# Performance work log

Measured on AMD Instinct MI355X. Metric: run time of the kernel, lower is better.

Reference implementation:

```python
import jax, jax.numpy as jnp
import numpy as np

B, S, H = 8, 512, 1024          # batch, seq_len, hidden_size
T, K, FF = 8, 2, 4096           # num_thoughts, top_k, ffn dim (4*H)
NH = 8                          # combiner attention heads
HD = H // NH
CREATIVITY = 1.0


def setup_inputs() -> dict:
    key = jax.random.key(0)
    ks = jax.random.split(key, 16)
    s = 0.02
    return {
        "hidden_states": jax.random.normal(ks[0], (B, S, H), jnp.float32),
        # router
        "router_w": jax.random.normal(ks[1], (H, T), jnp.float32) * s,
        "router_b": jnp.zeros((T,), jnp.float32),
        # thought branch FFNs (one per thought)
        "W1": jax.random.normal(ks[2], (T, H, FF), jnp.float32) * s,
        "b1": jnp.zeros((T, FF), jnp.float32),
        "W2": jax.random.normal(ks[3], (T, FF, H), jnp.float32) * s,
        "b2": jnp.zeros((T, H), jnp.float32),
        # attention combiner (MultiheadAttention proj weights)
        "Wq": jax.random.normal(ks[4], (H, H), jnp.float32) * s,
        "bq": jnp.zeros((H,), jnp.float32),
        "Wk": jax.random.normal(ks[5], (H, H), jnp.float32) * s,
        "bk": jnp.zeros((H,), jnp.float32),
        "Wv": jax.random.normal(ks[6], (H, H), jnp.float32) * s,
        "bv": jnp.zeros((H,), jnp.float32),
        "Wo": jax.random.normal(ks[7], (H, H), jnp.float32) * s,
        "bo": jnp.zeros((H,), jnp.float32),
    }


def reference(hidden_states, router_w, router_b, W1, b1, W2, b2,
              Wq, bq, Wk, bk, Wv, bv, Wo, bo):
    # ---- router: mean-pool -> linear -> softmax -> top-k ----
    pooled = hidden_states.mean(axis=1)                       # [B,H]
    router_probs = jax.nn.softmax(pooled @ router_w + router_b, axis=-1)  # [B,T]
    top_p, top_i = jax.lax.top_k(router_probs, K)             # [B,K]
    weights = jax.nn.softmax(top_p, axis=-1)                  # renormalized active weights [B,K]

    # ---- grouped branch FFN (gather expert weights, batched GEMMs) ----
    h = jnp.einsum('bsh,bkhf->bksf', hidden_states, W1[top_i]) + b1[top_i][:, :, None, :]
    h = jax.nn.gelu(h, approximate=False)
    branch_out = jnp.einsum('bksf,bkfh->bksh', h, W2[top_i]) + b2[top_i][:, :, None, :]
    branch_out = branch_out * CREATIVITY                      # [B,K,S,H]

    # ---- attention combiner over flattened thoughts [B, K*S, H] ----
    L = K * S
    flat = branch_out.reshape(B, L, H)
    q = (flat @ Wq + bq).reshape(B, L, NH, HD)
    k = (flat @ Wk + bk).reshape(B, L, NH, HD)
    v = (flat @ Wv + bv).reshape(B, L, NH, HD)
    scores = jnp.einsum('blhd,bmhd->bhlm', q, k) / jnp.sqrt(jnp.float32(HD))
    attn = jax.nn.softmax(scores, axis=-1)
    ctx = jnp.einsum('bhlm,bmhd->blhd', attn, v).reshape(B, L, H)
    attended = (ctx @ Wo + bo).reshape(B, K, S, H)

    combined = jnp.einsum('bksh,bk->bsh', attended, weights)  # [B,S,H]

    # ---- metrics ----
    entropy = jnp.mean(-jnp.sum(router_probs * jnp.log(router_probs + 1e-8), axis=1))
    a = branch_out[:, 0].reshape(B, -1)
    b_ = branch_out[:, 1].reshape(B, -1)
    cos = jnp.sum(a * b_, -1) / jnp.maximum(
        jnp.linalg.norm(a, axis=-1) * jnp.linalg.norm(b_, axis=-1), 1e-8)
    diversity = jnp.mean(1.0 - cos)
    return combined, entropy, diversity
```

## Files before the change

kernel.cpp:

```cpp
#include <hip/hip_runtime.h>
#include <hip/hip_bf16.h>
#include <math.h>

typedef float f32x4 __attribute__((ext_vector_type(4)));
typedef short s16x8 __attribute__((ext_vector_type(8)));
typedef short s16x4 __attribute__((ext_vector_type(4)));
typedef unsigned int u32;

#define DEVI __device__ __forceinline__

#define Bn   8
#define Sn   512
#define Hn   1024
#define Tn   8
#define Kn   2
#define FFn  4096
#define NHn  8
#define HDn  128
#define Ln   1024
#define OUT_COMBINED 4194304

DEVI unsigned short f2bf(float x) {
  __hip_bfloat16 h = __float2bfloat16(x);
  union { __hip_bfloat16 h; unsigned short u; } cv; cv.h = h; return cv.u;
}
DEVI float bf2f(unsigned short u) {
  union { u32 i; float f; } cv; cv.i = ((u32)u) << 16; return cv.f;
}

typedef __attribute__((address_space(3))) u32 lds_u32;
typedef __attribute__((address_space(1))) u32 glb_u32;
DEVI void gload16(const void* g, void* l) {
  __builtin_amdgcn_global_load_lds((const glb_u32*)g, (lds_u32*)l, 16, 0, 0);
}

__global__ __launch_bounds__(256) void pool_part_k(const float* __restrict__ hid, float* __restrict__ part)
{
  const int b = blockIdx.x, scn = blockIdx.y;
  const int hh = threadIdx.x * 4;
  float4 acc = make_float4(0.f, 0.f, 0.f, 0.f);
  const float* base = hid + ((long)b * Sn + (long)scn * 128) * Hn + hh;
  for (int s = 0; s < 128; ++s) {
    float4 v = *(const float4*)(base + (long)s * Hn);
    acc.x += v.x; acc.y += v.y; acc.z += v.z; acc.w += v.w;
  }
  *(float4*)(part + ((long)(scn * Bn + b)) * Hn + hh) = acc;
}

__global__ __launch_bounds__(256) void pool_final_k(const float* __restrict__ part, float* __restrict__ pooled)
{
  const int i = blockIdx.x * 256 + threadIdx.x;
  float s = 0.f;
  for (int sc = 0; sc < 4; ++sc) s += part[sc * (Bn * Hn) + i];
  pooled[i] = s * (1.f / (float)Sn);
}

__global__ __launch_bounds__(64) void router_k(
    const float* __restrict__ pooled, const float* __restrict__ rw, const float* __restrict__ rb,
    float* __restrict__ probs, int* __restrict__ topi, float* __restrict__ wts,
    int* __restrict__ flags, float* __restrict__ entropy_out)
{
  __shared__ float lg[64];
  __shared__ int sfl[8];
  __shared__ float sent[8];
  const int tid = threadIdx.x;
  const int b = tid >> 3, t = tid & 7;
  if (tid < 8) sfl[tid] = 0;
  float acc = rb[t];
  const float* pb = pooled + b * Hn;
  for (int i = 0; i < Hn; ++i) acc += pb[i] * rw[i * Tn + t];
  lg[tid] = acc;
  __syncthreads();
  if (t == 0) {
    float p[8];
    float mx = lg[b * 8];
    for (int i = 1; i < 8; ++i) mx = fmaxf(mx, lg[b * 8 + i]);
    float ssum = 0.f;
    for (int i = 0; i < 8; ++i) { p[i] = expf(lg[b * 8 + i] - mx); ssum += p[i]; }
    float ent = 0.f;
    for (int i = 0; i < 8; ++i) { p[i] /= ssum; ent -= p[i] * logf(p[i] + 1e-8f); probs[b * 8 + i] = p[i]; }
    sent[b] = ent;
    int i1 = 0;
    for (int i = 1; i < 8; ++i) if (p[i] > p[i1]) i1 = i;
    int i2 = (i1 == 0) ? 1 : 0;
    for (int i = 0; i < 8; ++i) if (i != i1 && p[i] > p[i2]) i2 = i;
    float w0 = 1.f / (1.f + expf(p[i2] - p[i1]));
    float w1 = 1.f / (1.f + expf(p[i1] - p[i2]));
    topi[b * 2] = i1; topi[b * 2 + 1] = i2;
    wts[b * 2] = w0; wts[b * 2 + 1] = w1;
    atomicOr(&sfl[i1], 1); atomicOr(&sfl[i2], 1);
  }
  __syncthreads();
  if (tid < 8) flags[tid] = sfl[tid];
  if (tid == 0) {
    float e = 0.f;
    for (int i = 0; i < 8; ++i) e += sent[i];
    entropy_out[0] = e * (1.f / (float)Bn);
  }
}

__global__ __launch_bounds__(256) void cvt_k(const float* __restrict__ in, unsigned short* __restrict__ out)
{
  const long i = ((long)blockIdx.x * 256 + threadIdx.x) * 4;
  float4 v = *(const float4*)(in + i);
  s16x4 o;
  o[0] = (short)f2bf(v.x); o[1] = (short)f2bf(v.y); o[2] = (short)f2bf(v.z); o[3] = (short)f2bf(v.w);
  *(s16x4*)(out + i) = o;
}

__global__ __launch_bounds__(256) void bias3_k(const float* __restrict__ bq, const float* __restrict__ bk,
                                               const float* __restrict__ bv, float* __restrict__ o)
{
  const int i = blockIdx.x * 256 + threadIdx.x;
  o[i] = bq[i]; o[i + 1024] = bk[i]; o[i + 2048] = bv[i];
}

__global__ __launch_bounds__(256) void transpose_k(const float* __restrict__ Win, unsigned short* __restrict__ Wout,
                                                   int Kd, int N, long sIn, long sOut, const int* __restrict__ flags)
{
  const int t = blockIdx.z;
  if (flags && flags[t] == 0) return;
  __shared__ float tile[64][65];
  const float* in = Win + (long)t * sIn;
  unsigned short* out = Wout + (long)t * sOut;
  const int kb = blockIdx.y * 64, nb = blockIdx.x * 64;
  const int tx = threadIdx.x & 15, ty = threadIdx.x >> 4;
  #pragma unroll
  for (int i = 0; i < 4; ++i) {
    const int r = ty + i * 16;
    float4 v = *(const float4*)(in + (long)(kb + r) * N + nb + tx * 4);
    tile[r][tx * 4 + 0] = v.x; tile[r][tx * 4 + 1] = v.y;
    tile[r][tx * 4 + 2] = v.z; tile[r][tx * 4 + 3] = v.w;
  }
  __syncthreads();
  #pragma unroll
  for (int i = 0; i < 4; ++i) {
    const int n = ty + i * 16;
    s16x4 o;
    #pragma unroll
    for (int j = 0; j < 4; ++j) o[j] = (short)f2bf(tile[tx * 4 + j][n]);
    *(s16x4*)(out + (long)(nb + n) * Kd + kb + tx * 4) = o;
  }
}

template<int EPI, int OUTMODE>
__global__ __launch_bounds__(256) void gemm_k(
    const unsigned short* __restrict__ A0, const unsigned short* __restrict__ Bt0,
    const float* __restrict__ bias0, unsigned short* __restrict__ C0,
    int N, int Kd,
    const int* __restrict__ topi, int kTop,
    long sA_b, long sA_p, long sBt_t, int sBias_t, long sC_p)
{
  __shared__ __align__(16) char smem[36864];
  const int z = blockIdx.z;
  const int bidx = kTop ? (z / kTop) : 0;
  const int t = topi ? topi[z] : 0;
  const unsigned short* A = A0 + (long)bidx * sA_b + (long)z * sA_p;
  const unsigned short* Bt = Bt0 + (long)t * sBt_t;
  const float* bias = bias0 + (long)t * sBias_t;
  unsigned short* C = C0 + (long)z * sC_p;

  const int m0 = blockIdx.y * 128;
  const int n0 = blockIdx.x * 128;
  const int tid = threadIdx.x;
  const int lane = tid & 63, w = tid >> 6;
  const int wm = w >> 1, wn = w & 1;

  const int srow = w * 32 + (lane >> 2);
  const int csw = ((lane & 3) ^ ((srow ^ (srow >> 2)) & 3)) << 4;

  const char* gA0 = (const char*)(A + (long)(m0 + srow) * Kd) + csw;
  const char* gA1 = (const char*)(A + (long)(m0 + srow + 16) * Kd) + csw;
  const char* gB0 = (const char*)(Bt + (long)(n0 + srow) * Kd) + csw;
  const char* gB1 = (const char*)(Bt + (long)(n0 + srow + 16) * Kd) + csw;

  char* ldsAw = smem + w * 2048;
  char* ldsBw = smem + 16384 + w * 2048;

  f32x4 acc[4][4];
  const f32x4 zero = {0.f, 0.f, 0.f, 0.f};
  #pragma unroll
  for (int i = 0; i < 4; ++i)
    #pragma unroll
    for (int j = 0; j < 4; ++j) acc[i][j] = zero;

  const int rA = lane & 15;
  const int cb = (lane >> 4) << 4;
  int aoff[4], boff[4];
  #pragma unroll
  for (int mi = 0; mi < 4; ++mi) {
    int row = wm * 64 + mi * 16 + rA;
    aoff[mi] = row * 64 + (cb ^ (((row ^ (row >> 2)) & 3) << 4));
    int rowb = wn * 64 + mi * 16 + rA;
    boff[mi] = rowb * 64 + (cb ^ (((rowb ^ (rowb >> 2)) & 3) << 4));
  }

  const int nIter = Kd >> 5;
  gload16(gA0, ldsAw);
  gload16(gA1, ldsAw + 1024);
  gload16(gB0, ldsBw);
  gload16(gB1, ldsBw + 1024);
  __syncthreads();

  int cur = 0;
  for (int it = 0; it < nIter; ++it) {
    if (it + 1 < nIter) {
      const long kb2 = (long)(it + 1) * 64;
      const int nb = cur ^ 1;
      gload16(gA0 + kb2, ldsAw + nb * 8192);
      gload16(gA1 + kb2, ldsAw + nb * 8192 + 1024);
      gload16(gB0 + kb2, ldsBw + nb * 8192);
      gload16(gB1 + kb2, ldsBw + nb * 8192 + 1024);
    }
    const char* pa = smem + cur * 8192;
    const char* pb = smem + 16384 + cur * 8192;
    s16x8 af[4], bfr[4];
    #pragma unroll
    for (int mi = 0; mi < 4; ++mi) af[mi] = *(const s16x8*)(pa + aoff[mi]);
    #pragma unroll
    for (int nj = 0; nj < 4; ++nj) bfr[nj] = *(const s16x8*)(pb + boff[nj]);
    __builtin_amdgcn_s_setprio(1);
    #pragma unroll
    for (int mi = 0; mi < 4; ++mi)
      #pragma unroll
      for (int nj = 0; nj < 4; ++nj)
        acc[mi][nj] = __builtin_amdgcn_mfma_f32_16x16x32_bf16(af[mi], bfr[nj], acc[mi][nj], 0, 0, 0);
    __builtin_amdgcn_s_setprio(0);
    __syncthreads();
    cur ^= 1;
  }

  unsigned short* et = (unsigned short*)(smem + w * 9216);
  const int r4 = (lane >> 4) << 2;
  const int nbase = n0 + wn * 64;
  const int seg = nbase >> 10;
  #pragma unroll
  for (int nj = 0; nj < 4; ++nj) {
    const int n = nbase + nj * 16 + rA;
    const float bv = bias[n];
    #pragma unroll
    for (int mi = 0; mi < 4; ++mi) {
      #pragma unroll
      for (int j = 0; j < 4; ++j) {
        float x = acc[mi][nj][j] + bv;
        if (EPI == 1) x = 0.5f * x * (1.0f + erff(x * 0.70710678118654752f));
        const int mrl = mi * 16 + r4 + j;
        const int ncl = nj * 16 + rA;
        if (OUTMODE == 0 || seg < 2) et[mrl * 72 + ncl] = f2bf(x);
        else                         et[ncl * 72 + mrl] = f2bf(x);
      }
    }
  }
  const int erow = lane >> 3, echunk = lane & 7;
  if (OUTMODE == 0) {
    const long r0 = m0 + wm * 64;
    #pragma unroll
    for (int rr = 0; rr < 8; ++rr) {
      const int row = rr * 8 + erow;
      s16x8 v = *(const s16x8*)(et + row * 72 + echunk * 8);
      *(s16x8*)(C + (r0 + row) * N + nbase + echunk * 8) = v;
    }
  } else {
    const int nseg = nbase & 1023;
    if (seg < 2) {
      unsigned short* dst = C + (long)seg * 8388608;
      const long r0 = m0 + wm * 64;
      #pragma unroll
      for (int rr = 0; rr < 8; ++rr) {
        const int row = rr * 8 + erow;
        s16x8 v = *(const s16x8*)(et + row * 72 + echunk * 8);
        *(s16x8*)(dst + (r0 + row) * 1024 + nseg + echunk * 8) = v;
      }
    } else {
      unsigned short* vtp = C + 16777216;
      const int bb = m0 >> 10;
      const int ltok0 = (m0 & 1023) + wm * 64;
      #pragma unroll
      for (int rr = 0; rr < 8; ++rr) {
        const int nrow = rr * 8 + erow;
        s16x8 v = *(const s16x8*)(et + nrow * 72 + echunk * 8);
        *(s16x8*)(vtp + ((long)(bb * 1024 + nseg + nrow)) * 1024 + ltok0 + echunk * 8) = v;
      }
    }
  }
}

__global__ __launch_bounds__(256) void flash_k(
    const unsigned short* __restrict__ q, const unsigned short* __restrict__ k,
    const unsigned short* __restrict__ vt, unsigned short* __restrict__ ctx)
{
  __shared__ unsigned short Ks[64 * 128];
  __shared__ unsigned short Vs[128 * 64];
  __shared__ unsigned short Ps[4][32 * 72];
  const int qt = blockIdx.x, h = blockIdx.y, b = blockIdx.z;
  const int tid = threadIdx.x, lane = tid & 63, w = tid >> 6;
  const int rA = lane & 15, g = lane >> 4;
  const int q0w = qt * 128 + w * 32;

  s16x8 qf[2][4];
  #pragma unroll
  for (int qi = 0; qi < 2; ++qi) {
    const unsigned short* qp = q + ((long)(b * Ln + q0w + qi * 16 + rA)) * Hn + h * HDn + g * 8;
    #pragma unroll
    for (int kk = 0; kk < 4; ++kk) qf[qi][kk] = *(const s16x8*)(qp + kk * 32);
  }

  f32x4 o[2][8];
  const f32x4 zero = {0.f, 0.f, 0.f, 0.f};
  #pragma unroll
  for (int qi = 0; qi < 2; ++qi)
    #pragma unroll
    for (int nn = 0; nn < 8; ++nn) o[qi][nn] = zero;
  float lrun[2][4];
  #pragma unroll
  for (int qi = 0; qi < 2; ++qi)
    #pragma unroll
    for (int j = 0; j < 4; ++j) lrun[qi][j] = 0.f;
  float m = 0.f;

  const float sc2 = 0.08838834764831845f * 1.4426950408889634f;

  const int krow0 = w * 16 + g;
  const int kc = lane & 15;
  const int vrow0 = w * 32 + (lane >> 3);
  const int vc = lane & 7;

  for (int kvt = 0; kvt < 16; ++kvt) {
    const int kv0 = kvt * 64;
    __syncthreads();
    #pragma unroll
    for (int qq = 0; qq < 4; ++qq) {
      const int rk = krow0 + qq * 4;
      gload16(k + ((long)(b * Ln + kv0 + rk)) * Hn + h * HDn + ((kc ^ (rk & 7)) * 8),
              (char*)Ks + w * 4096 + qq * 1024);
      const int rv = vrow0 + qq * 8;
      gload16(vt + ((long)(b * 1024 + h * HDn + rv)) * Ln + kv0 + ((vc ^ (rv & 7)) * 8),
              (char*)Vs + w * 4096 + qq * 1024);
    }
    __syncthreads();

    f32x4 sacc[2][4];
    #pragma unroll
    for (int qi = 0; qi < 2; ++qi)
      #pragma unroll
      for (int nj = 0; nj < 4; ++nj) sacc[qi][nj] = zero;
    #pragma unroll
    for (int kk = 0; kk < 4; ++kk) {
      #pragma unroll
      for (int nj = 0; nj < 4; ++nj) {
        const int row = nj * 16 + rA;
        const int byt = row * 256 + (((kk * 4 + g) ^ (row & 7)) << 4);
        s16x8 kf = *(const s16x8*)((const char*)Ks + byt);
        sacc[0][nj] = __builtin_amdgcn_mfma_f32_16x16x32_bf16(qf[0][kk], kf, sacc[0][nj], 0, 0, 0);
        sacc[1][nj] = __builtin_amdgcn_mfma_f32_16x16x32_bf16(qf[1][kk], kf, sacc[1][nj], 0, 0, 0);
      }
    }

    float vmax = -3.0e38f;
    #pragma unroll
    for (int qi = 0; qi < 2; ++qi)
      #pragma unroll
      for (int nj = 0; nj < 4; ++nj)
        #pragma unroll
        for (int j = 0; j < 4; ++j) {
          const float s = sacc[qi][nj][j] * sc2;
          sacc[qi][nj][j] = s;
          vmax = fmaxf(vmax, s);
        }
    if (!__all(vmax <= m + 8.0f)) {
      float mn = vmax;
      #pragma unroll
      for (int mm = 1; mm < 64; mm <<= 1) mn = fmaxf(mn, __shfl_xor(mn, mm, 64));
      const float al = exp2f(m - mn);
      #pragma unroll
      for (int qi = 0; qi < 2; ++qi) {
        #pragma unroll
        for (int nn = 0; nn < 8; ++nn)
          #pragma unroll
          for (int j = 0; j < 4; ++j) o[qi][nn][j] *= al;
        #pragma unroll
        for (int j = 0; j < 4; ++j) lrun[qi][j] *= al;
      }
      m = mn;
    }
    #pragma unroll
    for (int qi = 0; qi < 2; ++qi)
      #pragma unroll
      for (int j = 0; j < 4; ++j) {
        float p0 = exp2f(sacc[qi][0][j] - m);
        float p1 = exp2f(sacc[qi][1][j] - m);
        float p2 = exp2f(sacc[qi][2][j] - m);
        float p3 = exp2f(sacc[qi][3][j] - m);
        lrun[qi][j] += (p0 + p1) + (p2 + p3);
        const int prow = (qi * 16 + g * 4 + j) * 72;
        Ps[w][prow + 0 * 16 + rA] = f2bf(p0);
        Ps[w][prow + 1 * 16 + rA] = f2bf(p1);
        Ps[w][prow + 2 * 16 + rA] = f2bf(p2);
        Ps[w][prow + 3 * 16 + rA] = f2bf(p3);
      }

    s16x8 pf[2][2];
    #pragma unroll
    for (int qi = 0; qi < 2; ++qi)
      #pragma unroll
      for (int kk2 = 0; kk2 < 2; ++kk2)
        pf[qi][kk2] = *(const s16x8*)(&Ps[w][(qi * 16 + rA) * 72 + kk2 * 32 + g * 8]);
    #pragma unroll
    for (int kk2 = 0; kk2 < 2; ++kk2) {
      #pragma unroll
      for (int nn = 0; nn < 8; ++nn) {
        const int row = nn * 16 + rA;
        const int byt = row * 128 + (((kk2 * 4 + g) ^ (row & 7)) << 4);
        s16x8 vf = *(const s16x8*)((const char*)Vs + byt);
        o[0][nn] = __builtin_amdgcn_mfma_f32_16x16x32_bf16(pf[0][kk2], vf, o[0][nn], 0, 0, 0);
        o[1][nn] = __builtin_amdgcn_mfma_f32_16x16x32_bf16(pf[1][kk2], vf, o[1][nn], 0, 0, 0);
      }
    }
  }

  float linv[2][4];
  #pragma unroll
  for (int qi = 0; qi < 2; ++qi)
    #pragma unroll
    for (int j = 0; j < 4; ++j) {
      float l = lrun[qi][j];
      #pragma unroll
      for (int mm = 1; mm < 16; mm <<= 1) l += __shfl_xor(l, mm, 64);
      linv[qi][j] = 1.0f / l;
    }
  #pragma unroll
  for (int qi = 0; qi < 2; ++qi)
    #pragma unroll
    for (int nn = 0; nn < 8; ++nn)
      #pragma unroll
      for (int j = 0; j < 4; ++j) {
        const int row = q0w + qi * 16 + g * 4 + j;
        ctx[((long)(b * Ln + row)) * Hn + h * HDn + nn * 16 + rA] = f2bf(o[qi][nn][j] * linv[qi][j]);
      }
}

__global__ __launch_bounds__(256) void div_part_k(const unsigned short* __restrict__ br, float* __restrict__ part)
{
  const int b = blockIdx.y, ch = blockIdx.x;
  const unsigned short* a = br + (long)b * (2L * Sn * Hn);
  const unsigned short* c = a + (long)Sn * Hn;
  const int base = ch * 16384 + threadIdx.x * 8;
  float dot = 0.f, na = 0.f, nb = 0.f;
  #pragma unroll
  for (int i = 0; i < 8; ++i) {
    const int idx = base + i * 2048;
    s16x8 av = *(const s16x8*)(a + idx);
    s16x8 cv = *(const s16x8*)(c + idx);
    #pragma unroll
    for (int e = 0; e < 8; ++e) {
      float fa = bf2f((unsigned short)av[e]);
      float fc = bf2f((unsigned short)cv[e]);
      dot += fa * fc; na += fa * fa; nb += fc * fc;
    }
  }
  #pragma unroll
  for (int mm = 1; mm < 64; mm <<= 1) {
    dot += __shfl_xor(dot, mm, 64);
    na  += __shfl_xor(na, mm, 64);
    nb  += __shfl_xor(nb, mm, 64);
  }
  __shared__ float red[12];
  const int lane = threadIdx.x & 63, w = threadIdx.x >> 6;
  if (lane == 0) { red[w * 3] = dot; red[w * 3 + 1] = na; red[w * 3 + 2] = nb; }
  __syncthreads();
  if (threadIdx.x == 0) {
    float d = 0, x = 0, y = 0;
    for (int i = 0; i < 4; ++i) { d += red[i * 3]; x += red[i * 3 + 1]; y += red[i * 3 + 2]; }
    float* op = part + ((long)(b * 32 + ch)) * 3;
    op[0] = d; op[1] = x; op[2] = y;
  }
}

__global__ __launch_bounds__(64) void div_final_k(const float* __restrict__ part, float* __restrict__ outp)
{
  __shared__ float cosr[8];
  const int tid = threadIdx.x;
  if (tid < 8) {
    float d = 0, x = 0, y = 0;
    for (int i = 0; i < 32; ++i) {
      const float* p = part + ((long)(tid * 32 + i)) * 3;
      d += p[0]; x += p[1]; y += p[2];
    }
    cosr[tid] = d / fmaxf(sqrtf(x) * sqrtf(y), 1e-8f);
  }
  __syncthreads();
  if (tid == 0) {
    float s = 0.f;
    for (int i = 0; i < 8; ++i) s += 1.f - cosr[i];
    outp[0] = s * (1.f / 8.f);
  }
}

__global__ __launch_bounds__(256) void combine_k(const unsigned short* __restrict__ att,
                                                 const float* __restrict__ wts, float* __restrict__ out)
{
  const long i = ((long)blockIdx.x * 256 + threadIdx.x) * 8;
  const int b = (int)(i >> 19);
  const long rem = i & 524287;
  const unsigned short* a0 = att + (long)b * (2L * Sn * Hn) + rem;
  const unsigned short* a1 = a0 + (long)Sn * Hn;
  const float w0 = wts[b * 2], w1 = wts[b * 2 + 1];
  s16x8 v0 = *(const s16x8*)a0;
  s16x8 v1 = *(const s16x8*)a1;
  float r[8];
  #pragma unroll
  for (int e = 0; e < 8; ++e) r[e] = w0 * bf2f((unsigned short)v0[e]) + w1 * bf2f((unsigned short)v1[e]);
  *(float4*)(out + i)     = make_float4(r[0], r[1], r[2], r[3]);
  *(float4*)(out + i + 4) = make_float4(r[4], r[5], r[6], r[7]);
}

extern "C" void kernel_launch(void* const* d_in, const int* in_sizes, int n_in,
                              void* d_out, int out_size, void* d_ws, size_t ws_size,
                              hipStream_t stream)
{
  (void)in_sizes; (void)n_in; (void)out_size; (void)ws_size;
  const float* hidden   = (const float*)d_in[0];
  const float* router_w = (const float*)d_in[1];
  const float* router_b = (const float*)d_in[2];
  const float* W1 = (const float*)d_in[3];
  const float* b1 = (const float*)d_in[4];
  const float* W2 = (const float*)d_in[5];
  const float* b2 = (const float*)d_in[6];
  const float* Wq = (const float*)d_in[7];
  const float* bq = (const float*)d_in[8];
  const float* Wk = (const float*)d_in[9];
  const float* bk = (const float*)d_in[10];
  const float* Wv = (const float*)d_in[11];
  const float* bv = (const float*)d_in[12];
  const float* Wo = (const float*)d_in[13];
  const float* bo = (const float*)d_in[14];
  float* out = (float*)d_out;

  char* ws = (char*)d_ws;
  float* pooled  = (float*)(ws);
  float* ppart   = (float*)(ws + 32768);
  float* probs   = (float*)(ws + 163840);
  int*   topi    = (int*)  (ws + 164096);
  float* wts     = (float*)(ws + 164352);
  int*   flags   = (int*)  (ws + 164608);
  float* dpart   = (float*)(ws + 164864);
  float* qkvbias = (float*)(ws + 167936);
  unsigned short* hid_bf = (unsigned short*)(ws + 262144);
  unsigned short* Wt     = (unsigned short*)(ws + 262144 + 8388608);
  unsigned short* hbuf   = (unsigned short*)(ws + 262144 + 8388608 + 67108864);
  unsigned short* br     = (unsigned short*)(ws + 262144 + 8388608 + 134217728);
  unsigned short* wqkvo  = (unsigned short*)(ws + 262144 + 8388608 + 134217728 + 16777216);
  unsigned short* qb  = Wt;
  unsigned short* kbf = Wt + 8388608;
  unsigned short* vt  = Wt + 16777216;
  unsigned short* ctx = hbuf;
  unsigned short* att = hbuf + 8388608;
  unsigned short* wqt = wqkvo;
  unsigned short* wkt = wqkvo + 1048576;
  unsigned short* wvt = wqkvo + 2097152;
  unsigned short* wot = wqkvo + 3145728;

  pool_part_k<<<dim3(Bn, 4), 256, 0, stream>>>(hidden, ppart);
  pool_final_k<<<dim3(32), 256, 0, stream>>>(ppart, pooled);
  router_k<<<1, 64, 0, stream>>>(pooled, router_w, router_b, probs, topi, wts, flags, out + OUT_COMBINED);

  cvt_k<<<4096, 256, 0, stream>>>(hidden, hid_bf);
  bias3_k<<<4, 256, 0, stream>>>(bq, bk, bv, qkvbias);
  transpose_k<<<dim3(64, 16, Tn), 256, 0, stream>>>(W1, Wt, Hn, FFn, (long)Hn * FFn, (long)FFn * Hn, flags);
  transpose_k<<<dim3(16, 16, 1), 256, 0, stream>>>(Wq, wqt, Hn, Hn, 0, 0, nullptr);
  transpose_k<<<dim3(16, 16, 1), 256, 0, stream>>>(Wk, wkt, Hn, Hn, 0, 0, nullptr);
  transpose_k<<<dim3(16, 16, 1), 256, 0, stream>>>(Wv, wvt, Hn, Hn, 0, 0, nullptr);
  transpose_k<<<dim3(16, 16, 1), 256, 0, stream>>>(Wo, wot, Hn, Hn, 0, 0, nullptr);

  gemm_k<1, 0><<<dim3(FFn / 128, Sn / 128, 16), 256, 0, stream>>>(
      hid_bf, Wt, b1, hbuf, FFn, Hn, topi, 2,
      (long)Sn * Hn, 0L, (long)FFn * Hn, FFn, (long)Sn * FFn);

  transpose_k<<<dim3(16, 64, Tn), 256, 0, stream>>>(W2, Wt, FFn, Hn, (long)FFn * Hn, (long)Hn * FFn, flags);

  gemm_k<0, 0><<<dim3(Hn / 128, Sn / 128, 16), 256, 0, stream>>>(
      hbuf, Wt, b2, br, Hn, FFn, topi, 2,
      0L, (long)Sn * FFn, (long)Hn * FFn, Hn, (long)Sn * Hn);

  div_part_k<<<dim3(32, Bn), 256, 0, stream>>>(br, dpart);
  div_final_k<<<1, 64, 0, stream>>>(dpart, out + OUT_COMBINED + 1);

  gemm_k<0, 1><<<dim3(3072 / 128, (Bn * Ln) / 128, 1), 256, 0, stream>>>(
      br, wqkvo, qkvbias, qb, 3072, Hn, nullptr, 0, 0L, 0L, 0L, 0, 0L);

  flash_k<<<dim3(Ln / 128, NHn, Bn), 256, 0, stream>>>(qb, kbf, vt, ctx);

  gemm_k<0, 0><<<dim3(Hn / 128, (Bn * Ln) / 128, 1), 256, 0, stream>>>(
      ctx, wot, bo, att, Hn, Hn, nullptr, 0, 0L, 0L, 0L, 0, 0L);

  combine_k<<<2048, 256, 0, stream>>>(att, wts, out);
}
```

Measured before the change: 538.0 us.

## Replace 128x128 GEMM with 256-wide tiles and multi-stage LDS pipeline

Swaps the 128x128 double-buffered bf16 MFMA GEMM for a templated kernel with 256-wide N tiles and 256- or 128-row M tiles. It uses a 3-4 stage LDS ring with explicit vmcnt waits and global loads split across the two halves of each MFMA phase. The aim is more data reuse per tile and better overlap of memory with compute for the FFN, QKV and output GEMMs. The router's dot products are also split across 256 threads. In exchange, the larger tiles raise register and LDS use, and the hand-written waitcnt sequencing is fragile.

```diff
diff --git a/kernel.cpp b/kernel.cpp
--- a/kernel.cpp
+++ b/kernel.cpp
@@ -55,23 +55,27 @@
   pooled[i] = s * (1.f / (float)Sn);
 }
 
-__global__ __launch_bounds__(64) void router_k(
+__global__ __launch_bounds__(256) void router_k(
     const float* __restrict__ pooled, const float* __restrict__ rw, const float* __restrict__ rb,
     float* __restrict__ probs, int* __restrict__ topi, float* __restrict__ wts,
     int* __restrict__ flags, float* __restrict__ entropy_out)
 {
+  __shared__ float partial[256];
   __shared__ float lg[64];
   __shared__ int sfl[8];
   __shared__ float sent[8];
   const int tid = threadIdx.x;
-  const int b = tid >> 3, t = tid & 7;
+  const int bt = tid & 63, slice = tid >> 6;
+  const int b = bt >> 3, t = bt & 7;
   if (tid < 8) sfl[tid] = 0;
-  float acc = rb[t];
+  float acc = 0.f;
   const float* pb = pooled + b * Hn;
-  for (int i = 0; i < Hn; ++i) acc += pb[i] * rw[i * Tn + t];
-  lg[tid] = acc;
+  for (int i = slice * 256; i < slice * 256 + 256; ++i) acc += pb[i] * rw[i * Tn + t];
+  partial[tid] = acc;
   __syncthreads();
-  if (t == 0) {
+  if (tid < 64) lg[tid] = rb[t] + partial[tid] + partial[tid + 64] + partial[tid + 128] + partial[tid + 192];
+  __syncthreads();
+  if (tid < 64 && t == 0) {
     float p[8];
     float mx = lg[b * 8];
     for (int i = 1; i < 8; ++i) mx = fmaxf(mx, lg[b * 8 + i]);
@@ -143,143 +147,208 @@
   }
 }
 
-template<int EPI, int OUTMODE>
-__global__ __launch_bounds__(256) void gemm_k(
+template<int WM, int EPI, int OUTMODE>
+__global__ __launch_bounds__(WM * 256, 2) void gemm256_k(
     const unsigned short* __restrict__ A0, const unsigned short* __restrict__ Bt0,
     const float* __restrict__ bias0, unsigned short* __restrict__ C0,
     int N, int Kd,
     const int* __restrict__ topi, int kTop,
     long sA_b, long sA_p, long sBt_t, int sBias_t, long sC_p)
 {
-  __shared__ __align__(16) char smem[36864];
+  constexpr int NBUF = (WM == 2) ? 4 : 3;
+  constexpr int ASZ = WM * 8192;
+  constexpr int BSZ = 16384;
+  constexpr int BISS = 4 / WM;
+  __shared__ __align__(16) char smem[NBUF * (ASZ + BSZ)];
+  char* const Ab = smem;
+  char* const Bb = smem + NBUF * ASZ;
+
   const int z = blockIdx.z;
   const int bidx = kTop ? (z / kTop) : 0;
-  const int t = topi ? topi[z] : 0;
+  const int te = topi ? topi[z] : 0;
   const unsigned short* A = A0 + (long)bidx * sA_b + (long)z * sA_p;
-  const unsigned short* Bt = Bt0 + (long)t * sBt_t;
-  const float* bias = bias0 + (long)t * sBias_t;
+  const unsigned short* Bt = Bt0 + (long)te * sBt_t;
+  const float* bias = bias0 + (long)te * sBias_t;
   unsigned short* C = C0 + (long)z * sC_p;
 
-  const int m0 = blockIdx.y * 128;
-  const int n0 = blockIdx.x * 128;
+  const int m0 = blockIdx.y * (WM * 128);
+  const int n0 = blockIdx.x * 256;
   const int tid = threadIdx.x;
   const int lane = tid & 63, w = tid >> 6;
-  const int wm = w >> 1, wn = w & 1;
-
-  const int srow = w * 32 + (lane >> 2);
-  const int csw = ((lane & 3) ^ ((srow ^ (srow >> 2)) & 3)) << 4;
-
-  const char* gA0 = (const char*)(A + (long)(m0 + srow) * Kd) + csw;
-  const char* gA1 = (const char*)(A + (long)(m0 + srow + 16) * Kd) + csw;
-  const char* gB0 = (const char*)(Bt + (long)(n0 + srow) * Kd) + csw;
-  const char* gB1 = (const char*)(Bt + (long)(n0 + srow + 16) * Kd) + csw;
-
-  char* ldsAw = smem + w * 2048;
-  char* ldsBw = smem + 16384 + w * 2048;
-
-  f32x4 acc[4][4];
+  const int wm = w >> 2, wn = w & 3;
+  const int rA = lane & 15, g = lane >> 4;
+
+  const int srow = tid >> 2;
+  const int sc   = tid & 3;
+  const unsigned short* gA[2];
+  #pragma unroll
+  for (int i = 0; i < 2; ++i) {
+    const int r = i * (WM * 64) + srow;
+    gA[i] = A + (long)(m0 + r) * Kd + ((sc ^ ((r >> 1) & 3)) * 8);
+  }
+  const unsigned short* gB[BISS];
+  #pragma unroll
+  for (int i = 0; i < BISS; ++i) {
+    const int r = i * (WM * 64) + srow;
+    gB[i] = Bt + (long)(n0 + r) * Kd + ((sc ^ ((r >> 1) & 3)) * 8);
+  }
+  const int sdo = tid * 16;
+
+  int aoff[8], boff[4];
+  #pragma unroll
+  for (int mi = 0; mi < 8; ++mi) {
+    const int row = wm * 128 + mi * 16 + rA;
+    aoff[mi] = row * 64 + ((g ^ ((row >> 1) & 3)) << 4);
+  }
+  #pragma unroll
+  for (int nj = 0; nj < 4; ++nj) {
+    const int row = wn * 64 + nj * 16 + rA;
+    boff[nj] = row * 64 + ((g ^ ((row >> 1) & 3)) << 4);
+  }
+
+  f32x4 acc[8][4];
   const f32x4 zero = {0.f, 0.f, 0.f, 0.f};
   #pragma unroll
-  for (int i = 0; i < 4; ++i)
+  for (int i = 0; i < 8; ++i)
     #pragma unroll
     for (int j = 0; j < 4; ++j) acc[i][j] = zero;
 
-  const int rA = lane & 15;
-  const int cb = (lane >> 4) << 4;
-  int aoff[4], boff[4];
-  #pragma unroll
-  for (int mi = 0; mi < 4; ++mi) {
-    int row = wm * 64 + mi * 16 + rA;
-    aoff[mi] = row * 64 + (cb ^ (((row ^ (row >> 2)) & 3) << 4));
-    int rowb = wn * 64 + mi * 16 + rA;
-    boff[mi] = rowb * 64 + (cb ^ (((rowb ^ (rowb >> 2)) & 3) << 4));
-  }
-
-  const int nIter = Kd >> 5;
-  gload16(gA0, ldsAw);
-  gload16(gA1, ldsAw + 1024);
-  gload16(gB0, ldsBw);
-  gload16(gB1, ldsBw + 1024);
+  const int nt = Kd >> 5;
+
+  for (int j = 0; j < NBUF - 1; ++j) {
+    #pragma unroll
+    for (int i = 0; i < 2; ++i)
+      gload16(gA[i] + j * 32, Ab + j * ASZ + i * (WM * 4096) + sdo);
+    #pragma unroll
+    for (int i = 0; i < BISS; ++i)
+      gload16(gB[i] + j * 32, Bb + j * BSZ + i * (WM * 4096) + sdo);
+  }
+  if constexpr (WM == 2) asm volatile("s_waitcnt vmcnt(8)" ::: "memory");
+  else                   asm volatile("s_waitcnt vmcnt(6)" ::: "memory");
+  __builtin_amdgcn_s_barrier();
+
+  int cb = 0;
+  for (int kt = 0; kt < nt; ++kt) {
+    const char* pa = Ab + cb * ASZ;
+    const char* pb = Bb + cb * BSZ;
+    const int ft = kt + NBUF - 1;
+    const int fb = (cb == 0) ? NBUF - 1 : cb - 1;
+    const bool st = (ft < nt);
+
+    s16x8 af[4], bf[4];
+    #pragma unroll
+    for (int mi = 0; mi < 4; ++mi) af[mi] = *(const s16x8*)(pa + aoff[mi]);
+    #pragma unroll
+    for (int nj = 0; nj < 4; ++nj) bf[nj] = *(const s16x8*)(pb + boff[nj]);
+    if (st) {
+      #pragma unroll
+      for (int i = 0; i < 2; ++i)
+        gload16(gA[i] + ft * 32, Ab + fb * ASZ + i * (WM * 4096) + sdo);
+      if constexpr (WM == 1)
+        gload16(gB[0] + ft * 32, Bb + fb * BSZ + sdo);
+    }
+    asm volatile("" ::: "memory");
+    __builtin_amdgcn_s_barrier();
+    __builtin_amdgcn_s_setprio(1);
+    #pragma unroll
+    for (int mi = 0; mi < 4; ++mi)
+      #pragma unroll
+      for (int nj = 0; nj < 4; ++nj)
+        acc[mi][nj] = __builtin_amdgcn_mfma_f32_16x16x32_bf16(af[mi], bf[nj], acc[mi][nj], 0, 0, 0);
+    __builtin_amdgcn_s_setprio(0);
+    __builtin_amdgcn_s_barrier();
+
+    s16x8 af2[4];
+    #pragma unroll
+    for (int mi = 0; mi < 4; ++mi) af2[mi] = *(const s16x8*)(pa + aoff[4 + mi]);
+    if (st) {
+      if constexpr (WM == 2) {
+        gload16(gB[0] + ft * 32, Bb + fb * BSZ + sdo);
+        gload16(gB[1] + ft * 32, Bb + fb * BSZ + 8192 + sdo);
+      } else {
+        gload16(gB[1] + ft * 32, Bb + fb * BSZ + 4096 + sdo);
+        gload16(gB[2] + ft * 32, Bb + fb * BSZ + 8192 + sdo);
+        gload16(gB[3] + ft * 32, Bb + fb * BSZ + 12288 + sdo);
+      }
+    }
+    asm volatile("" ::: "memory");
+    __builtin_amdgcn_s_barrier();
+    __builtin_amdgcn_s_setprio(1);
+    #pragma unroll
+    for (int mi = 0; mi < 4; ++mi)
+      #pragma unroll
+      for (int nj = 0; nj < 4; ++nj)
+        acc[4 + mi][nj] = __builtin_amdgcn_mfma_f32_16x16x32_bf16(af2[mi], bf[nj], acc[4 + mi][nj], 0, 0, 0);
+    __builtin_amdgcn_s_setprio(0);
+
+    if constexpr (WM == 2) {
+      if (kt < nt - 3)       asm volatile("s_waitcnt vmcnt(8)" ::: "memory");
+      else if (kt == nt - 3) asm volatile("s_waitcnt vmcnt(4)" ::: "memory");
+      else if (kt == nt - 2) asm volatile("s_waitcnt vmcnt(0)" ::: "memory");
+    } else {
+      if (kt < nt - 2)       asm volatile("s_waitcnt vmcnt(6)" ::: "memory");
+      else if (kt == nt - 2) asm volatile("s_waitcnt vmcnt(0)" ::: "memory");
+    }
+    __builtin_amdgcn_s_barrier();
+    cb = (cb + 1 == NBUF) ? 0 : cb + 1;
+  }
+
   __syncthreads();
-
-  int cur = 0;
-  for (int it = 0; it < nIter; ++it) {
-    if (it + 1 < nIter) {
-      const long kb2 = (long)(it + 1) * 64;
-      const int nb = cur ^ 1;
-      gload16(gA0 + kb2, ldsAw + nb * 8192);
-      gload16(gA1 + kb2, ldsAw + nb * 8192 + 1024);
-      gload16(gB0 + kb2, ldsBw + nb * 8192);
-      gload16(gB1 + kb2, ldsBw + nb * 8192 + 1024);
-    }
-    const char* pa = smem + cur * 8192;
-    const char* pb = smem + 16384 + cur * 8192;
-    s16x8 af[4], bfr[4];
-    #pragma unroll
-    for (int mi = 0; mi < 4; ++mi) af[mi] = *(const s16x8*)(pa + aoff[mi]);
-    #pragma unroll
-    for (int nj = 0; nj < 4; ++nj) bfr[nj] = *(const s16x8*)(pb + boff[nj]);
-    __builtin_amdgcn_s_setprio(1);
-    #pragma unroll
-    for (int mi = 0; mi < 4; ++mi)
-      #pragma unroll
-      for (int nj = 0; nj < 4; ++nj)
-        acc[mi][nj] = __builtin_amdgcn_mfma_f32_16x16x32_bf16(af[mi], bfr[nj], acc[mi][nj], 0, 0, 0);
-    __builtin_amdgcn_s_setprio(0);
-    __syncthreads();
-    cur ^= 1;
-  }
 
   unsigned short* et = (unsigned short*)(smem + w * 9216);
   const int r4 = (lane >> 4) << 2;
   const int nbase = n0 + wn * 64;
-  const int seg = nbase >> 10;
-  #pragma unroll
-  for (int nj = 0; nj < 4; ++nj) {
-    const int n = nbase + nj * 16 + rA;
-    const float bv = bias[n];
-    #pragma unroll
-    for (int mi = 0; mi < 4; ++mi) {
-      #pragma unroll
-      for (int j = 0; j < 4; ++j) {
-        float x = acc[mi][nj][j] + bv;
-        if (EPI == 1) x = 0.5f * x * (1.0f + erff(x * 0.70710678118654752f));
-        const int mrl = mi * 16 + r4 + j;
-        const int ncl = nj * 16 + rA;
-        if (OUTMODE == 0 || seg < 2) et[mrl * 72 + ncl] = f2bf(x);
-        else                         et[ncl * 72 + mrl] = f2bf(x);
-      }
-    }
-  }
+  const int seg = (OUTMODE == 1) ? (nbase >> 10) : 0;
   const int erow = lane >> 3, echunk = lane & 7;
-  if (OUTMODE == 0) {
-    const long r0 = m0 + wm * 64;
-    #pragma unroll
-    for (int rr = 0; rr < 8; ++rr) {
-      const int row = rr * 8 + erow;
-      s16x8 v = *(const s16x8*)(et + row * 72 + echunk * 8);
-      *(s16x8*)(C + (r0 + row) * N + nbase + echunk * 8) = v;
-    }
-  } else {
-    const int nseg = nbase & 1023;
-    if (seg < 2) {
-      unsigned short* dst = C + (long)seg * 8388608;
-      const long r0 = m0 + wm * 64;
+  float bv[4];
+  #pragma unroll
+  for (int nj = 0; nj < 4; ++nj) bv[nj] = bias[nbase + nj * 16 + rA];
+
+  #pragma unroll
+  for (int p = 0; p < 2; ++p) {
+    #pragma unroll
+    for (int nj = 0; nj < 4; ++nj) {
+      #pragma unroll
+      for (int mi2 = 0; mi2 < 4; ++mi2) {
+        #pragma unroll
+        for (int j = 0; j < 4; ++j) {
+          float x = acc[p * 4 + mi2][nj][j] + bv[nj];
+          if (EPI == 1) x = 0.5f * x * (1.0f + erff(x * 0.70710678118654752f));
+          const int mrl = mi2 * 16 + r4 + j;
+          const int ncl = nj * 16 + rA;
+          if (OUTMODE == 0 || seg < 2) et[mrl * 72 + ncl] = f2bf(x);
+          else                         et[ncl * 72 + mrl] = f2bf(x);
+        }
+      }
+    }
+    const long mrow0 = m0 + wm * 128 + p * 64;
+    if (OUTMODE == 0) {
       #pragma unroll
       for (int rr = 0; rr < 8; ++rr) {
         const int row = rr * 8 + erow;
         s16x8 v = *(const s16x8*)(et + row * 72 + echunk * 8);
-        *(s16x8*)(dst + (r0 + row) * 1024 + nseg + echunk * 8) = v;
+        *(s16x8*)(C + (mrow0 + row) * N + nbase + echunk * 8) = v;
       }
     } else {
-      unsigned short* vtp = C + 16777216;
-      const int bb = m0 >> 10;
-      const int ltok0 = (m0 & 1023) + wm * 64;
-      #pragma unroll
-      for (int rr = 0; rr < 8; ++rr) {
-        const int nrow = rr * 8 + erow;
-        s16x8 v = *(const s16x8*)(et + nrow * 72 + echunk * 8);
-        *(s16x8*)(vtp + ((long)(bb * 1024 + nseg + nrow)) * 1024 + ltok0 + echunk * 8) = v;
+      const int nseg = nbase & 1023;
+      if (seg < 2) {
+        unsigned short* dst = C + (long)seg * 8388608;
+        #pragma unroll
+        for (int rr = 0; rr < 8; ++rr) {
+          const int row = rr * 8 + erow;
+          s16x8 v = *(const s16x8*)(et + row * 72 + echunk * 8);
+          *(s16x8*)(dst + (mrow0 + row) * 1024 + nseg + echunk * 8) = v;
+        }
+      } else {
+        unsigned short* vtp = C + 16777216;
+        const int bb = (int)(mrow0 >> 10);
+        const int ltok0 = (int)(mrow0 & 1023);
+        #pragma unroll
+        for (int rr = 0; rr < 8; ++rr) {
+          const int nrow = rr * 8 + erow;
+          s16x8 v = *(const s16x8*)(et + nrow * 72 + echunk * 8);
+          *(s16x8*)(vtp + ((long)(bb * 1024 + nseg + nrow)) * 1024 + ltok0 + echunk * 8) = v;
+        }
       }
     }
   }
@@ -562,7 +631,7 @@
 
   pool_part_k<<<dim3(Bn, 4), 256, 0, stream>>>(hidden, ppart);
   pool_final_k<<<dim3(32), 256, 0, stream>>>(ppart, pooled);
-  router_k<<<1, 64, 0, stream>>>(pooled, router_w, router_b, probs, topi, wts, flags, out + OUT_COMBINED);
+  router_k<<<1, 256, 0, stream>>>(pooled, router_w, router_b, probs, topi, wts, flags, out + OUT_COMBINED);
 
   cvt_k<<<4096, 256, 0, stream>>>(hidden, hid_bf);
   bias3_k<<<4, 256, 0, stream>>>(bq, bk, bv, qkvbias);
@@ -572,25 +641,25 @@
   transpose_k<<<dim3(16, 16, 1), 256, 0, stream>>>(Wv, wvt, Hn, Hn, 0, 0, nullptr);
   transpose_k<<<dim3(16, 16, 1), 256, 0, stream>>>(Wo, wot, Hn, Hn, 0, 0, nullptr);
 
-  gemm_k<1, 0><<<dim3(FFn / 128, Sn / 128, 16), 256, 0, stream>>>(
+  gemm256_k<2, 1, 0><<<dim3(FFn / 256, Sn / 256, 16), 512, 0, stream>>>(
       hid_bf, Wt, b1, hbuf, FFn, Hn, topi, 2,
       (long)Sn * Hn, 0L, (long)FFn * Hn, FFn, (long)Sn * FFn);
 
   transpose_k<<<dim3(16, 64, Tn), 256, 0, stream>>>(W2, Wt, FFn, Hn, (long)FFn * Hn, (long)Hn * FFn, flags);
 
-  gemm_k<0, 0><<<dim3(Hn / 128, Sn / 128, 16), 256, 0, stream>>>(
+  gemm256_k<1, 0, 0><<<dim3(Hn / 256, Sn / 128, 16), 256, 0, stream>>>(
       hbuf, Wt, b2, br, Hn, FFn, topi, 2,
       0L, (long)Sn * FFn, (long)Hn * FFn, Hn, (long)Sn * Hn);
 
   div_part_k<<<dim3(32, Bn), 256, 0, stream>>>(br, dpart);
   div_final_k<<<1, 64, 0, stream>>>(dpart, out + OUT_COMBINED + 1);
 
-  gemm_k<0, 1><<<dim3(3072 / 128, (Bn * Ln) / 128, 1), 256, 0, stream>>>(
+  gemm256_k<2, 0, 1><<<dim3(3072 / 256, (Bn * Ln) / 256, 1), 512, 0, stream>>>(
       br, wqkvo, qkvbias, qb, 3072, Hn, nullptr, 0, 0L, 0L, 0L, 0, 0L);
 
   flash_k<<<dim3(Ln / 128, NHn, Bn), 256, 0, stream>>>(qb, kbf, vt, ctx);
 
-  gemm_k<0, 0><<<dim3(Hn / 128, (Bn * Ln) / 128, 1), 256, 0, stream>>>(
+  gemm256_k<1, 0, 0><<<dim3(Hn / 256, (Bn * Ln) / 128, 1), 256, 0, stream>>>(
       ctx, wot, bo, att, Hn, Hn, nullptr, 0, 0L, 0L, 0L, 0, 0L);
 
   combine_k<<<2048, 256, 0, stream>>>(att, wts, out);
```

Result: no change. 536.6 us (-0.3%).
